# Kernel tuning notes

Hardware: AMD Instinct MI355X
Metric: run time of the kernel (lower is better)

Reference implementation:

```python
import jax, jax.numpy as jnp
import numpy as np

N_NODES = 20000
N_EDGES = 100000
NODE_IN = 16
EDGE_IN = 10
LEAK = 0.1
EPS = 1e-5


def setup_inputs() -> dict:
    key = jax.random.key(0)
    ks = iter(jax.random.split(key, 40))

    def rn(shape, scale):
        return jax.random.normal(next(ks), shape, dtype=jnp.float32) * scale

    inp = {}
    inp["x"] = jax.random.normal(next(ks), (N_NODES, NODE_IN), dtype=jnp.float32)
    inp["e"] = jax.random.normal(next(ks), (N_EDGES, EDGE_IN), dtype=jnp.float32)
    inp["edge_index"] = jax.random.randint(next(ks), (2, N_EDGES), 0, N_NODES, dtype=jnp.int64)
    inp["xbatch"] = jnp.zeros((N_NODES,), dtype=jnp.int64)

    # BatchNorm affine params
    inp["bn_node_g"] = jnp.ones((NODE_IN,), jnp.float32)
    inp["bn_node_b"] = jnp.zeros((NODE_IN,), jnp.float32)
    inp["bn_edge_g"] = jnp.ones((EDGE_IN,), jnp.float32)
    inp["bn_edge_b"] = jnp.zeros((EDGE_IN,), jnp.float32)

    # nn1: Lin(10,16) -> LeakyReLU -> Lin(16, 16*32) -> LeakyReLU
    inp["nn1_w1"] = rn((EDGE_IN, 16), 0.3); inp["nn1_b1"] = jnp.zeros((16,), jnp.float32)
    inp["nn1_w2"] = rn((16, 16 * 32), 0.25); inp["nn1_b2"] = jnp.zeros((16 * 32,), jnp.float32)
    # nn2: Lin(10,32) -> LeakyReLU -> Lin(32, 32*64) -> LeakyReLU
    inp["nn2_w1"] = rn((EDGE_IN, 32), 0.3); inp["nn2_b1"] = jnp.zeros((32,), jnp.float32)
    inp["nn2_w2"] = rn((32, 32 * 64), 0.18); inp["nn2_b2"] = jnp.zeros((32 * 64,), jnp.float32)

    # NNConv root weights + biases
    inp["l1_root"] = rn((16, 32), 0.25); inp["l1_bias"] = jnp.zeros((32,), jnp.float32)
    inp["l2_root"] = rn((32, 64), 0.18); inp["l2_bias"] = jnp.zeros((64,), jnp.float32)

    # edge_pred_mlp: 138 -> 64 -> 32 -> 16 -> 8 -> 2
    dims = [2 * 64 + EDGE_IN, 64, 32, 16, 8, 2]
    for i in range(5):
        inp[f"mlp_w{i+1}"] = rn((dims[i], dims[i + 1]), 1.0 / np.sqrt(dims[i]))
        inp[f"mlp_b{i+1}"] = jnp.zeros((dims[i + 1],), jnp.float32)
    return inp


def _bn(v, g, b):
    # BatchNorm1d, training-mode batch statistics (biased variance), eps=1e-5
    m = v.mean(axis=0)
    var = v.var(axis=0)
    return (v - m) * jax.lax.rsqrt(var + EPS) * g + b


def _lrelu(v):
    return jax.nn.leaky_relu(v, LEAK)


def _nnconv(x, src, dst, e, w1, b1, w2, b2, root, bias, c_in, c_out):
    # edge MLP -> per-edge weight matrix [E, c_in, c_out]
    h = _lrelu(e @ w1 + b1)
    W = _lrelu(h @ w2 + b2).reshape(-1, c_in, c_out)
    # gather source features, per-edge matmul, scatter-add to targets
    msg = jnp.einsum("ei,eio->eo", x[src], W)
    agg = jax.ops.segment_sum(msg, dst, num_segments=x.shape[0])
    return agg + x @ root + bias


def reference(x, e, edge_index, xbatch,
              bn_node_g, bn_node_b, bn_edge_g, bn_edge_b,
              nn1_w1, nn1_b1, nn1_w2, nn1_b2,
              nn2_w1, nn2_b1, nn2_w2, nn2_b2,
              l1_root, l1_bias, l2_root, l2_bias,
              mlp_w1, mlp_b1, mlp_w2, mlp_b2, mlp_w3, mlp_b3,
              mlp_w4, mlp_b4, mlp_w5, mlp_b5):
    src, dst = edge_index[0], edge_index[1]
    e = _bn(e, bn_edge_g, bn_edge_b)
    x = _bn(x, bn_node_g, bn_node_b)
    x = _nnconv(x, src, dst, e, nn1_w1, nn1_b1, nn1_w2, nn1_b2, l1_root, l1_bias, 16, 32)
    x = _nnconv(x, src, dst, e, nn2_w1, nn2_b1, nn2_w2, nn2_b2, l2_root, l2_bias, 32, 64)
    # MetaLayer edge model: cat(source, target, edge_attr) -> MLP -> [E, 2]
    h = jnp.concatenate([x[src], x[dst], e], axis=1)
    h = _lrelu(h @ mlp_w1 + mlp_b1)
    h = _lrelu(h @ mlp_w2 + mlp_b2)
    h = _lrelu(h @ mlp_w3 + mlp_b3)
    h = _lrelu(h @ mlp_w4 + mlp_b4)
    edge_pred = h @ mlp_w5 + mlp_b5
    return edge_pred
```

## Files before the change

kernel.cpp:

```cpp
#include <hip/hip_runtime.h>
#include <cstdint>

#define N_NODES 20000
#define N_EDGES 100000
#define BN_EPS 1e-5f

typedef __attribute__((ext_vector_type(8))) short short8;
typedef __attribute__((ext_vector_type(4))) float floatx4;
typedef __attribute__((ext_vector_type(2))) float float2v;

__device__ __forceinline__ float lrelu(float v) { return fmaxf(v, 0.1f * v); }
__device__ __forceinline__ float4 ld4(const float* p) { return *reinterpret_cast<const float4*>(p); }
__device__ __forceinline__ float2 ld2(const float* p) { return *reinterpret_cast<const float2*>(p); }

__device__ __forceinline__ void atomAddF(float* p, float v) {
#if defined(__HIP_DEVICE_COMPILE__)
    unsafeAtomicAdd(p, v);
#else
    atomicAdd(p, v);
#endif
}

__device__ __forceinline__ unsigned short f2bf(float f) {
    union { float f; uint32_t u; } v; v.f = f;
    uint32_t r = v.u + 0x7fffu + ((v.u >> 16) & 1u);
    return (unsigned short)(r >> 16);
}
__device__ __forceinline__ uint32_t pack2(float a, float b) {
    return (uint32_t)f2bf(a) | ((uint32_t)f2bf(b) << 16);
}
__device__ __forceinline__ short8 pack8(float4 a, float4 b) {
    union { short8 s; uint32_t u[4]; } r;
    r.u[0] = pack2(a.x, a.y); r.u[1] = pack2(a.z, a.w);
    r.u[2] = pack2(b.x, b.y); r.u[3] = pack2(b.z, b.w);
    return r.s;
}

__device__ void stats10_dev(const float* __restrict__ v, int rows, float* __restrict__ out,
                            int blk, int nblk, float* sh) {
    if (threadIdx.x < 20) sh[threadIdx.x] = 0.f;
    __syncthreads();
    int nf2 = rows * 5;
    int stride = nblk * 256;
    int g = blk * 256 + threadIdx.x;
    int c2 = g % 5;
    float s0 = 0.f, s1 = 0.f, q0 = 0.f, q1 = 0.f;
    const float2* p = reinterpret_cast<const float2*>(v);
    for (int i = g; i < nf2; i += stride) {
        float2 t = p[i];
        s0 += t.x; s1 += t.y; q0 += t.x * t.x; q1 += t.y * t.y;
    }
    atomicAdd(&sh[2 * c2], s0);
    atomicAdd(&sh[2 * c2 + 1], s1);
    atomicAdd(&sh[10 + 2 * c2], q0);
    atomicAdd(&sh[10 + 2 * c2 + 1], q1);
    __syncthreads();
    if (threadIdx.x < 20) atomAddF(&out[threadIdx.x], sh[threadIdx.x]);
}

__device__ void stats16_dev(const float* __restrict__ v, int rows, float* __restrict__ out,
                            int blk, int nblk, float* sh) {
    if (threadIdx.x < 32) sh[threadIdx.x] = 0.f;
    __syncthreads();
    int nf4 = rows * 4;
    int stride = nblk * 256;
    int g = blk * 256 + threadIdx.x;
    int cg = (g & 3) * 4;
    float s[4] = {0.f, 0.f, 0.f, 0.f}, q[4] = {0.f, 0.f, 0.f, 0.f};
    const float4* p = reinterpret_cast<const float4*>(v);
    for (int i = g; i < nf4; i += stride) {
        float4 t = p[i];
        s[0] += t.x; s[1] += t.y; s[2] += t.z; s[3] += t.w;
        q[0] += t.x * t.x; q[1] += t.y * t.y; q[2] += t.z * t.z; q[3] += t.w * t.w;
    }
    #pragma unroll
    for (int off = 32; off >= 4; off >>= 1) {
        #pragma unroll
        for (int j = 0; j < 4; ++j) {
            s[j] += __shfl_down(s[j], off, 64);
            q[j] += __shfl_down(q[j], off, 64);
        }
    }
    if ((threadIdx.x & 63) < 4) {
        #pragma unroll
        for (int j = 0; j < 4; ++j) {
            atomicAdd(&sh[cg + j], s[j]);
            atomicAdd(&sh[16 + cg + j], q[j]);
        }
    }
    __syncthreads();
    if (threadIdx.x < 32) atomAddF(&out[threadIdx.x], sh[threadIdx.x]);
}

template<int CIN, int COUT, int H, int OCH>
__device__ void convpack_row(const float* __restrict__ w2, const float* __restrict__ b2,
                             char* __restrict__ pk, int r) {
    constexpr int NROW = CIN * OCH;
    constexpr int WB = NROW * 64;
    constexpr int PACKB = WB + NROW * 4;
    if (r >= CIN * COUT) return;
    int chunk = r / NROW;
    int rem = r % NROW;
    int i = rem / OCH, ol = rem % OCH;
    int n = i * COUT + chunk * OCH + ol;
    char* base = pk + (size_t)chunk * PACKB;
    uint32_t pkv[16];
    #pragma unroll
    for (int t = 0; t < 16; ++t) pkv[t] = 0;
    #pragma unroll
    for (int k = 0; k < H; k += 2)
        pkv[k >> 1] = pack2(w2[(size_t)k * (CIN * COUT) + n],
                            w2[(size_t)(k + 1) * (CIN * COUT) + n]);
    uint4* ob = reinterpret_cast<uint4*>(base);
    #pragma unroll
    for (int q = 0; q < 4; ++q)
        ob[(size_t)q * NROW + rem] = make_uint4(pkv[4 * q], pkv[4 * q + 1],
                                                pkv[4 * q + 2], pkv[4 * q + 3]);
    ((float*)(base + WB))[rem] = b2[n];
}

#define P1_S10 120
#define P1_S16 120
__global__ __launch_bounds__(256)
void prep1_kernel(const float* __restrict__ e, const float* __restrict__ x,
                  float* __restrict__ stats_e, float* __restrict__ stats_x,
                  const int* __restrict__ dst, int* __restrict__ counts,
                  const float* __restrict__ nn1_w2, const float* __restrict__ nn1_b2, char* __restrict__ cpack1,
                  const float* __restrict__ nn2_w2, const float* __restrict__ nn2_b2, char* __restrict__ cpack2,
                  const float* __restrict__ mw1, unsigned short* __restrict__ w1t,
                  const float* __restrict__ mw2, const float* __restrict__ mb2,
                  const float* __restrict__ mw3, const float* __restrict__ mb3,
                  const float* __restrict__ mw4, const float* __restrict__ mb4,
                  const float* __restrict__ mw5, const float* __restrict__ mb5,
                  float* __restrict__ mlpw)
{
    __shared__ float sh[32];
    int b = blockIdx.x;
    if (b < P1_S10) {
        stats10_dev(e, N_EDGES, stats_e, b, P1_S10, sh);
    } else if (b < P1_S10 + P1_S16) {
        stats16_dev(x, N_NODES, stats_x, b - P1_S10, P1_S16, sh);
    } else if (b < 631) {
        int i = (b - 240) * 256 + threadIdx.x;
        if (i < N_EDGES) atomicAdd(&counts[dst[i]], 1);
    } else if (b < 633) {
        convpack_row<16, 32, 16, 32>(nn1_w2, nn1_b2, cpack1, (b - 631) * 256 + threadIdx.x);
    } else if (b < 641) {
        convpack_row<32, 64, 32, 16>(nn2_w2, nn2_b2, cpack2, (b - 633) * 256 + threadIdx.x);
    } else {
        if (threadIdx.x < 64) {
            int o = threadIdx.x;
            for (int k = 0; k < 160; k += 2) {
                float a = (k < 138) ? mw1[(size_t)k * 64 + o] : 0.f;
                float c = (k + 1 < 138) ? mw1[(size_t)(k + 1) * 64 + o] : 0.f;
                *reinterpret_cast<uint32_t*>(w1t + (size_t)o * 160 + k) = pack2(a, c);
            }
        }
        for (int i = threadIdx.x; i < 2764; i += 256) {
            float v = 0.f;
            if (i < 2048) v = mw2[i];
            else if (i < 2560) v = mw3[i - 2048];
            else if (i < 2688) v = mw4[i - 2560];
            else if (i < 2704) v = mw5[i - 2688];
            else if (i < 2736) v = mb2[i - 2704];
            else if (i < 2752) v = mb3[i - 2736];
            else if (i < 2760) v = mb4[i - 2752];
            else if (i < 2762) v = mb5[i - 2760];
            mlpw[i] = v;
        }
    }
}

__global__ void scan_kernel(const int* __restrict__ counts, int* __restrict__ starts,
                            int* __restrict__ cursor, int n) {
    __shared__ int wsum[4];
    const int CH = (n + 255) / 256;
    int t = threadIdx.x;
    int lane = t & 63, wv = t >> 6;
    int lo = t * CH, hi = min(lo + CH, n);
    int s = 0;
    for (int i = lo; i < hi; ++i) s += counts[i];
    int v = s;
    #pragma unroll
    for (int off = 1; off < 64; off <<= 1) {
        int u = __shfl_up(v, off, 64);
        if (lane >= off) v += u;
    }
    if (lane == 63) wsum[wv] = v;
    __syncthreads();
    int woff = 0;
    for (int w = 0; w < wv; ++w) woff += wsum[w];
    int acc = woff + v - s;
    for (int i = lo; i < hi; ++i) {
        starts[i] = acc; cursor[i] = acc; acc += counts[i];
    }
}

#define P2_N16 1250
#define P2_SCAT 391
#define P2_HGEN 391
__global__ __launch_bounds__(256)
void prep2_kernel(const float* __restrict__ x, const float* __restrict__ stats_x,
                  const float* __restrict__ bn_node_g, const float* __restrict__ bn_node_b,
                  float* __restrict__ x_n,
                  const int* __restrict__ dst, int* __restrict__ cursor, int* __restrict__ epos,
                  const float* __restrict__ e, const float* __restrict__ stats_e,
                  const float* __restrict__ bn_edge_g, const float* __restrict__ bn_edge_b,
                  float* __restrict__ e_n,
                  const float* __restrict__ w1a, const float* __restrict__ b1a,
                  const float* __restrict__ w1b, const float* __restrict__ b1b,
                  unsigned short* __restrict__ h1, unsigned short* __restrict__ h2)
{
    int b = blockIdx.x;
    if (b < P2_N16) {
        int idx = b * 256 + threadIdx.x;
        if (idx >= N_NODES * 16) return;
        int c = idx & 15;
        float N = (float)N_NODES;
        float m = stats_x[c] / N;
        float var = stats_x[16 + c] / N - m * m;
        float sc = rsqrtf(var + BN_EPS) * bn_node_g[c];
        x_n[idx] = (x[idx] - m) * sc + bn_node_b[c];
    } else if (b < P2_N16 + P2_SCAT) {
        int i = (b - P2_N16) * 256 + threadIdx.x;
        if (i < N_EDGES) {
            int p = atomicAdd(&cursor[dst[i]], 1);
            epos[i] = p;
        }
    } else {
        int eg = (b - P2_N16 - P2_SCAT) * 256 + threadIdx.x;
        if (eg >= N_EDGES) return;
        float ev[10];
        float Ecnt = (float)N_EDGES;
        #pragma unroll
        for (int j = 0; j < 10; ++j) {
            float m = stats_e[j] / Ecnt;
            float var = stats_e[10 + j] / Ecnt - m * m;
            float sc = rsqrtf(var + BN_EPS) * bn_edge_g[j];
            ev[j] = (e[(size_t)eg * 10 + j] - m) * sc + bn_edge_b[j];
            e_n[(size_t)eg * 10 + j] = ev[j];
        }
        {
            uint32_t pk[16];
            #pragma unroll
            for (int t = 0; t < 16; ++t) pk[t] = 0;
            #pragma unroll
            for (int k = 0; k < 16; k += 2) {
                float a0 = b1a[k], a1 = b1a[k + 1];
                #pragma unroll
                for (int j = 0; j < 10; ++j) {
                    a0 += ev[j] * w1a[j * 16 + k];
                    a1 += ev[j] * w1a[j * 16 + k + 1];
                }
                pk[k >> 1] = pack2(lrelu(a0), lrelu(a1));
            }
            uint4* o = reinterpret_cast<uint4*>(h1 + (size_t)eg * 32);
            o[0] = make_uint4(pk[0], pk[1], pk[2], pk[3]);
            o[1] = make_uint4(pk[4], pk[5], pk[6], pk[7]);
            o[2] = make_uint4(pk[8], pk[9], pk[10], pk[11]);
            o[3] = make_uint4(pk[12], pk[13], pk[14], pk[15]);
        }
        {
            uint32_t pk[16];
            #pragma unroll
            for (int k = 0; k < 32; k += 2) {
                float a0 = b1b[k], a1 = b1b[k + 1];
                #pragma unroll
                for (int j = 0; j < 10; ++j) {
                    a0 += ev[j] * w1b[j * 32 + k];
                    a1 += ev[j] * w1b[j * 32 + k + 1];
                }
                pk[k >> 1] = pack2(lrelu(a0), lrelu(a1));
            }
            uint4* o = reinterpret_cast<uint4*>(h2 + (size_t)eg * 32);
            o[0] = make_uint4(pk[0], pk[1], pk[2], pk[3]);
            o[1] = make_uint4(pk[4], pk[5], pk[6], pk[7]);
            o[2] = make_uint4(pk[8], pk[9], pk[10], pk[11]);
            o[3] = make_uint4(pk[12], pk[13], pk[14], pk[15]);
        }
    }
}

template<int CIN, int COUT, int OCH, int NE>
__global__ __launch_bounds__(256, 4)
void conv_lds_kernel(const unsigned short* __restrict__ hbuf,
                     const char* __restrict__ pack,
                     const int* __restrict__ src,
                     const int* __restrict__ epos,
                     const float* __restrict__ xin,
                     float* __restrict__ msgbuf,
                     int n_edges)
{
    constexpr int NCH = COUT / OCH;
    constexpr int NROW = CIN * OCH;
    constexpr int WB = NROW * 64;
    constexpr int PACKB = WB + NROW * 4;
    __shared__ char smem[PACKB];

    int tid = threadIdx.x;
    int chunk = blockIdx.x % NCH;
    int eblk = blockIdx.x / NCH;

    {
        const uint4* g = reinterpret_cast<const uint4*>(pack + (size_t)chunk * PACKB);
        uint4* s = reinterpret_cast<uint4*>(smem);
        #pragma unroll 1
        for (int o = tid; o < PACKB / 16; o += 256) s[o] = g[o];
    }
    __syncthreads();

    int wv = tid >> 6, lane = tid & 63;
    int el = lane & 15, quad = lane >> 4;
    int g0 = (eblk * 4 + wv) * NE;

    const unsigned short* wlds = reinterpret_cast<const unsigned short*>(smem)
                                 + ((size_t)quad * NROW + el) * 8;
    const float* blds = reinterpret_cast<const float*>(smem + WB) + quad * 4;

    const float2v pt = {0.1f, 0.1f};

    #pragma unroll 1
    for (int gI = 0; gI < NE; ++gI) {
        int e0 = (g0 + gI) * 16;
        if (e0 >= n_edges) return;
        int e = e0 + el;
        int s = src[e];
        int slot = epos[e];

        short8 bfrag = *reinterpret_cast<const short8*>(hbuf + (size_t)e * 32 + quad * 8);

        float xr[CIN];
        #pragma unroll
        for (int i = 0; i < CIN; i += 4) {
            float4 v = ld4(xin + (size_t)s * CIN + i);
            xr[i] = v.x; xr[i + 1] = v.y; xr[i + 2] = v.z; xr[i + 3] = v.w;
        }

        float2v msg0[OCH / 16], msg1[OCH / 16];
        #pragma unroll
        for (int t = 0; t < OCH / 16; ++t) {
            msg0[t] = (float2v){0.f, 0.f};
            msg1[t] = (float2v){0.f, 0.f};
        }

        #pragma unroll 8
        for (int i = 0; i < CIN; ++i) {
            float2v xi2 = {xr[i], xr[i]};
            #pragma unroll
            for (int ot = 0; ot < OCH / 16; ++ot) {
                short8 af = *reinterpret_cast<const short8*>(wlds + (i * OCH + ot * 16) * 8);
                float4 bb = *reinterpret_cast<const float4*>(blds + i * OCH + ot * 16);
                floatx4 c = {bb.x, bb.y, bb.z, bb.w};
                c = __builtin_amdgcn_mfma_f32_16x16x32_bf16(af, bfrag, c, 0, 0, 0);
                float2v c0 = {c[0], c[1]};
                float2v c1 = {c[2], c[3]};
                float2v m0 = __builtin_elementwise_max(c0, c0 * pt);
                float2v m1 = __builtin_elementwise_max(c1, c1 * pt);
                msg0[ot] += xi2 * m0;
                msg1[ot] += xi2 * m1;
            }
        }

        float* orow = msgbuf + (size_t)slot * COUT + chunk * OCH;
        #pragma unroll
        for (int ot = 0; ot < OCH / 16; ++ot)
            *reinterpret_cast<float4*>(orow + ot * 16 + quad * 4) =
                make_float4(msg0[ot][0], msg0[ot][1], msg1[ot][0], msg1[ot][1]);
    }
}

template<int CIN, int C>
__global__ __launch_bounds__(256)
void gather_root_kernel(const float* __restrict__ xin, const float* __restrict__ w,
                        const float* __restrict__ bias,
                        const float* __restrict__ msg,
                        const int* __restrict__ starts, const int* __restrict__ counts,
                        float* __restrict__ xout, int nodes)
{
    constexpr int NPW = 64 / C;
    int wv = blockIdx.x * 4 + (threadIdx.x >> 6);
    int lane = threadIdx.x & 63;
    int node = wv * NPW + lane / C;
    int ch = lane % C;
    if (node >= nodes) return;
    float acc = bias[ch];
    const float* xrow = xin + (size_t)node * CIN;
    #pragma unroll
    for (int i = 0; i < CIN; ++i) acc += xrow[i] * w[i * C + ch];
    int s0 = starts[node], cnt = counts[node];
    const float* mrow = msg + (size_t)s0 * C + ch;
    int i = 0;
    for (; i + 3 < cnt; i += 4) {
        float m0 = mrow[(size_t)(i)     * C];
        float m1 = mrow[(size_t)(i + 1) * C];
        float m2 = mrow[(size_t)(i + 2) * C];
        float m3 = mrow[(size_t)(i + 3) * C];
        acc += (m0 + m1) + (m2 + m3);
    }
    for (; i < cnt; ++i) acc += mrow[(size_t)i * C];
    xout[(size_t)node * C + ch] = acc;
}

__global__ __launch_bounds__(256)
void mlp2_kernel(const float* __restrict__ x2, const float* __restrict__ e_n,
                 const int* __restrict__ src, const int* __restrict__ dst,
                 const unsigned short* __restrict__ w1t, const float* __restrict__ b1,
                 const float* __restrict__ mlpw,
                 float* __restrict__ out, int n_edges)
{
    __shared__ float wl[2764];
    __shared__ float a1t[4 * 1092];
    __shared__ float a2scr[4 * 528];

    int tid = threadIdx.x;
    {
        const uint4* g = reinterpret_cast<const uint4*>(mlpw);
        uint4* s = reinterpret_cast<uint4*>(wl);
        #pragma unroll 1
        for (int i = tid; i < 691; i += 256) s[i] = g[i];
    }

    int wv = tid >> 6, lane = tid & 63;
    int el = lane & 15, quad = lane >> 4;
    int e = blockIdx.x * 64 + wv * 16 + el;
    int eS = (e < n_edges) ? e : (n_edges - 1);
    int sN = src[eS], dN = dst[eS];

    short8 bf[5];
    {
        const float* rs = x2 + (size_t)sN * 64 + quad * 8;
        const float* rd = x2 + (size_t)dN * 64 + quad * 8;
        bf[0] = pack8(ld4(rs), ld4(rs + 4));
        bf[1] = pack8(ld4(rs + 32), ld4(rs + 36));
        bf[2] = pack8(ld4(rd), ld4(rd + 4));
        bf[3] = pack8(ld4(rd + 32), ld4(rd + 36));
        union { short8 s; uint32_t u[4]; } t;
        t.u[0] = t.u[1] = t.u[2] = t.u[3] = 0;
        const float* ep = e_n + (size_t)eS * 10;
        if (quad == 0) {
            float2 p0 = ld2(ep), p1 = ld2(ep + 2), p2 = ld2(ep + 4), p3 = ld2(ep + 6);
            t.u[0] = pack2(p0.x, p0.y); t.u[1] = pack2(p1.x, p1.y);
            t.u[2] = pack2(p2.x, p2.y); t.u[3] = pack2(p3.x, p3.y);
        } else if (quad == 1) {
            float2 p4 = ld2(ep + 8);
            t.u[0] = pack2(p4.x, p4.y);
        }
        bf[4] = t.s;
    }

    float* slab = &a1t[wv * 1092];
    {
        floatx4 acc[4];
        #pragma unroll
        for (int ot = 0; ot < 4; ++ot) {
            float4 bb = ld4(b1 + ot * 16 + quad * 4);
            acc[ot] = (floatx4){bb.x, bb.y, bb.z, bb.w};
        }
        #pragma unroll
        for (int ks = 0; ks < 5; ++ks) {
            #pragma unroll
            for (int ot = 0; ot < 4; ++ot) {
                short8 af = *reinterpret_cast<const short8*>(
                    w1t + (size_t)(ot * 16 + el) * 160 + ks * 32 + quad * 8);
                acc[ot] = __builtin_amdgcn_mfma_f32_16x16x32_bf16(af, bf[ks], acc[ot], 0, 0, 0);
            }
        }
        #pragma unroll
        for (int ot = 0; ot < 4; ++ot) {
            #pragma unroll
            for (int r = 0; r < 4; ++r)
                slab[(ot * 16 + quad * 4 + r) * 17 + el] = lrelu(acc[ot][r]);
        }
    }
    __syncthreads();

    const float* w2l = wl;            const float* w3l = wl + 2048;
    const float* w4l = wl + 2560;     const float* w5l = wl + 2688;
    const float* b2l = wl + 2704;     const float* b3l = wl + 2736;
    const float* b4l = wl + 2752;     const float* b5l = wl + 2760;
    float* a2s = &a2scr[wv * 528];
    float* a3s = slab;
    float* a4s = slab + 512;
    int p = quad;

    {
        float a2[8];
        #pragma unroll
        for (int j = 0; j < 8; ++j) a2[j] = b2l[p * 8 + j];
        #pragma unroll 4
        for (int i = 0; i < 64; ++i) {
            float ai = slab[i * 17 + el];
            #pragma unroll
            for (int j = 0; j < 8; ++j) a2[j] += ai * w2l[i * 32 + p * 8 + j];
        }
        #pragma unroll
        for (int j = 0; j < 8; ++j) a2s[el * 33 + p * 8 + j] = lrelu(a2[j]);
    }
    {
        float a3[4];
        #pragma unroll
        for (int j = 0; j < 4; ++j) a3[j] = b3l[p * 4 + j];
        #pragma unroll 4
        for (int i = 0; i < 32; ++i) {
            float ai = a2s[el * 33 + i];
            #pragma unroll
            for (int j = 0; j < 4; ++j) a3[j] += ai * w3l[i * 16 + p * 4 + j];
        }
        #pragma unroll
        for (int j = 0; j < 4; ++j) a3s[el * 17 + p * 4 + j] = lrelu(a3[j]);
    }
    {
        float a4[2];
        a4[0] = b4l[p * 2]; a4[1] = b4l[p * 2 + 1];
        #pragma unroll
        for (int i = 0; i < 16; ++i) {
            float ai = a3s[el * 17 + i];
            a4[0] += ai * w4l[i * 8 + p * 2];
            a4[1] += ai * w4l[i * 8 + p * 2 + 1];
        }
        a4s[el * 9 + p * 2]     = lrelu(a4[0]);
        a4s[el * 9 + p * 2 + 1] = lrelu(a4[1]);
    }
    if (p < 2) {
        float o = b5l[p];
        #pragma unroll
        for (int i = 0; i < 8; ++i) o += a4s[el * 9 + i] * w5l[i * 2 + p];
        if (e < n_edges) out[(size_t)e * 2 + p] = o;
    }
}

extern "C" void kernel_launch(void* const* d_in, const int* in_sizes, int n_in,
                              void* d_out, int out_size, void* d_ws, size_t ws_size,
                              hipStream_t stream)
{
    const float* x  = (const float*)d_in[0];
    const float* e  = (const float*)d_in[1];
    const int*   ei = (const int*)d_in[2];
    const float* bn_node_g = (const float*)d_in[4];
    const float* bn_node_b = (const float*)d_in[5];
    const float* bn_edge_g = (const float*)d_in[6];
    const float* bn_edge_b = (const float*)d_in[7];
    const float* nn1_w1 = (const float*)d_in[8];
    const float* nn1_b1 = (const float*)d_in[9];
    const float* nn1_w2 = (const float*)d_in[10];
    const float* nn1_b2 = (const float*)d_in[11];
    const float* nn2_w1 = (const float*)d_in[12];
    const float* nn2_b1 = (const float*)d_in[13];
    const float* nn2_w2 = (const float*)d_in[14];
    const float* nn2_b2 = (const float*)d_in[15];
    const float* l1_root = (const float*)d_in[16];
    const float* l1_bias = (const float*)d_in[17];
    const float* l2_root = (const float*)d_in[18];
    const float* l2_bias = (const float*)d_in[19];
    const float* mw1 = (const float*)d_in[20]; const float* mb1 = (const float*)d_in[21];
    const float* mw2 = (const float*)d_in[22]; const float* mb2 = (const float*)d_in[23];
    const float* mw3 = (const float*)d_in[24]; const float* mb3 = (const float*)d_in[25];
    const float* mw4 = (const float*)d_in[26]; const float* mb4 = (const float*)d_in[27];
    const float* mw5 = (const float*)d_in[28]; const float* mb5 = (const float*)d_in[29];

    const int* src = ei;
    const int* dst = ei + N_EDGES;

    float* ws = (float*)d_ws;
    float* stats_e = ws;
    float* stats_x = ws + 32;
    int* counts = (int*)(ws + 64);
    int* starts = counts + 20000;
    int* cursor = starts + 20000;
    int* epos   = cursor + 20000;
    float* e_n = ws + 64 + 160000;
    float* x_n = e_n + 1000000;
    float* x1  = x_n + 320000;
    float* x2  = x1 + 640000;
    float* msg = x2 + 1280000;
    unsigned short* h1   = (unsigned short*)(msg + 6400000);
    unsigned short* h2   = h1 + 3200000;
    unsigned short* w1t  = h2 + 3200000;
    char* cpack1 = (char*)(w1t + 10240);
    char* cpack2 = cpack1 + 34816;
    float* mlpw = (float*)(cpack2 + 4 * 34816);
    float* out = (float*)d_out;

    (void)hipMemsetAsync(d_ws, 0, (64 + 20000) * 4, stream);

    prep1_kernel<<<642, 256, 0, stream>>>(
        e, x, stats_e, stats_x, dst, counts,
        nn1_w2, nn1_b2, cpack1, nn2_w2, nn2_b2, cpack2,
        mw1, w1t, mw2, mb2, mw3, mb3, mw4, mb4, mw5, mb5, mlpw);

    scan_kernel<<<1, 256, 0, stream>>>(counts, starts, cursor, N_NODES);

    prep2_kernel<<<P2_N16 + P2_SCAT + P2_HGEN, 256, 0, stream>>>(
        x, stats_x, bn_node_g, bn_node_b, x_n,
        dst, cursor, epos,
        e, stats_e, bn_edge_g, bn_edge_b, e_n,
        nn1_w1, nn1_b1, nn2_w1, nn2_b1, h1, h2);

    const int NGRP = (N_EDGES + 15) / 16;
    const int CB = (NGRP + 15) / 16;

    conv_lds_kernel<16, 32, 32, 4><<<CB, 256, 0, stream>>>(h1, cpack1, src, epos, x_n, msg, N_EDGES);
    gather_root_kernel<16, 32><<<(N_NODES / 2 + 3) / 4, 256, 0, stream>>>(
        x_n, l1_root, l1_bias, msg, starts, counts, x1, N_NODES);

    conv_lds_kernel<32, 64, 16, 4><<<CB * 4, 256, 0, stream>>>(h2, cpack2, src, epos, x1, msg, N_EDGES);
    gather_root_kernel<32, 64><<<(N_NODES + 3) / 4, 256, 0, stream>>>(
        x1, l2_root, l2_bias, msg, starts, counts, x2, N_NODES);

    mlp2_kernel<<<(N_EDGES + 63) / 64, 256, 0, stream>>>(
        x2, e_n, src, dst, w1t, mb1, mlpw, out, N_EDGES);
}
```

Baseline: 336.1 us.

## Interchange conv loop to reuse LDS weight fragments across edge groups

The per-edge conv kernel now processes all NE edge groups of a wave together. Each LDS weight/bias fragment is loaded once and fed to NE independent MFMAs instead of being reloaded per group. Source indices, slots and h fragments are preloaded up front, and node features are fetched in IB-sized blocks. This cuts LDS traffic and exposes more independent MFMA work, but raises register pressure under the 4-blocks-per-CU launch bound.

```diff
diff --git a/kernel.cpp b/kernel.cpp
--- a/kernel.cpp
+++ b/kernel.cpp
@@ -281,7 +281,7 @@
     }
 }
 
-template<int CIN, int COUT, int OCH, int NE>
+template<int CIN, int COUT, int OCH, int NE, int IB>
 __global__ __launch_bounds__(256, 4)
 void conv_lds_kernel(const unsigned short* __restrict__ hbuf,
                      const char* __restrict__ pack,
@@ -295,6 +295,7 @@
     constexpr int NROW = CIN * OCH;
     constexpr int WB = NROW * 64;
     constexpr int PACKB = WB + NROW * 4;
+    constexpr int NOT = OCH / 16;
     __shared__ char smem[PACKB];
 
     int tid = threadIdx.x;
@@ -312,60 +313,75 @@
     int wv = tid >> 6, lane = tid & 63;
     int el = lane & 15, quad = lane >> 4;
     int g0 = (eblk * 4 + wv) * NE;
+    if (g0 * 16 >= n_edges) return;
 
     const unsigned short* wlds = reinterpret_cast<const unsigned short*>(smem)
                                  + ((size_t)quad * NROW + el) * 8;
     const float* blds = reinterpret_cast<const float*>(smem + WB) + quad * 4;
 
+    int sg[NE], slot[NE];
+    short8 bfrag[NE];
+    #pragma unroll
+    for (int g = 0; g < NE; ++g) {
+        int e0 = (g0 + g) * 16;
+        int e = (e0 < n_edges) ? (e0 + el) : el;
+        sg[g] = src[e];
+        slot[g] = epos[e];
+        bfrag[g] = *reinterpret_cast<const short8*>(hbuf + (size_t)e * 32 + quad * 8);
+    }
+
+    float2v msg0[NE][NOT], msg1[NE][NOT];
+    #pragma unroll
+    for (int g = 0; g < NE; ++g)
+        #pragma unroll
+        for (int t = 0; t < NOT; ++t) {
+            msg0[g][t] = (float2v){0.f, 0.f};
+            msg1[g][t] = (float2v){0.f, 0.f};
+        }
+
     const float2v pt = {0.1f, 0.1f};
 
     #pragma unroll 1
-    for (int gI = 0; gI < NE; ++gI) {
-        int e0 = (g0 + gI) * 16;
-        if (e0 >= n_edges) return;
-        int e = e0 + el;
-        int s = src[e];
-        int slot = epos[e];
-
-        short8 bfrag = *reinterpret_cast<const short8*>(hbuf + (size_t)e * 32 + quad * 8);
-
-        float xr[CIN];
-        #pragma unroll
-        for (int i = 0; i < CIN; i += 4) {
-            float4 v = ld4(xin + (size_t)s * CIN + i);
-            xr[i] = v.x; xr[i + 1] = v.y; xr[i + 2] = v.z; xr[i + 3] = v.w;
-        }
-
-        float2v msg0[OCH / 16], msg1[OCH / 16];
-        #pragma unroll
-        for (int t = 0; t < OCH / 16; ++t) {
-            msg0[t] = (float2v){0.f, 0.f};
-            msg1[t] = (float2v){0.f, 0.f};
-        }
-
-        #pragma unroll 8
-        for (int i = 0; i < CIN; ++i) {
-            float2v xi2 = {xr[i], xr[i]};
-            #pragma unroll
-            for (int ot = 0; ot < OCH / 16; ++ot) {
+    for (int ib = 0; ib < CIN / IB; ++ib) {
+        float xs[NE][IB];
+        #pragma unroll
+        for (int g = 0; g < NE; ++g) {
+            #pragma unroll
+            for (int t = 0; t < IB; t += 4) {
+                float4 v = ld4(xin + (size_t)sg[g] * CIN + ib * IB + t);
+                xs[g][t] = v.x; xs[g][t + 1] = v.y; xs[g][t + 2] = v.z; xs[g][t + 3] = v.w;
+            }
+        }
+        #pragma unroll
+        for (int ii = 0; ii < IB; ++ii) {
+            int i = ib * IB + ii;
+            #pragma unroll
+            for (int ot = 0; ot < NOT; ++ot) {
                 short8 af = *reinterpret_cast<const short8*>(wlds + (i * OCH + ot * 16) * 8);
                 float4 bb = *reinterpret_cast<const float4*>(blds + i * OCH + ot * 16);
-                floatx4 c = {bb.x, bb.y, bb.z, bb.w};
-                c = __builtin_amdgcn_mfma_f32_16x16x32_bf16(af, bfrag, c, 0, 0, 0);
-                float2v c0 = {c[0], c[1]};
-                float2v c1 = {c[2], c[3]};
-                float2v m0 = __builtin_elementwise_max(c0, c0 * pt);
-                float2v m1 = __builtin_elementwise_max(c1, c1 * pt);
-                msg0[ot] += xi2 * m0;
-                msg1[ot] += xi2 * m1;
+                floatx4 cinit = {bb.x, bb.y, bb.z, bb.w};
+                #pragma unroll
+                for (int g = 0; g < NE; ++g) {
+                    floatx4 c = __builtin_amdgcn_mfma_f32_16x16x32_bf16(af, bfrag[g], cinit, 0, 0, 0);
+                    float2v c0 = {c[0], c[1]}, c1 = {c[2], c[3]};
+                    float2v m0 = __builtin_elementwise_max(c0, c0 * pt);
+                    float2v m1 = __builtin_elementwise_max(c1, c1 * pt);
+                    float2v xi2 = {xs[g][ii], xs[g][ii]};
+                    msg0[g][ot] += xi2 * m0;
+                    msg1[g][ot] += xi2 * m1;
+                }
             }
         }
-
-        float* orow = msgbuf + (size_t)slot * COUT + chunk * OCH;
-        #pragma unroll
-        for (int ot = 0; ot < OCH / 16; ++ot)
+    }
+
+    #pragma unroll
+    for (int g = 0; g < NE; ++g) {
+        if ((g0 + g) * 16 >= n_edges) break;
+        float* orow = msgbuf + (size_t)slot[g] * COUT + chunk * OCH;
+        #pragma unroll
+        for (int ot = 0; ot < NOT; ++ot)
             *reinterpret_cast<float4*>(orow + ot * 16 + quad * 4) =
-                make_float4(msg0[ot][0], msg0[ot][1], msg1[ot][0], msg1[ot][1]);
+                make_float4(msg0[g][ot][0], msg0[g][ot][1], msg1[g][ot][0], msg1[g][ot][1]);
     }
 }
 
@@ -599,11 +615,11 @@
     const int NGRP = (N_EDGES + 15) / 16;
     const int CB = (NGRP + 15) / 16;
 
-    conv_lds_kernel<16, 32, 32, 4><<<CB, 256, 0, stream>>>(h1, cpack1, src, epos, x_n, msg, N_EDGES);
+    conv_lds_kernel<16, 32, 32, 4, 4><<<CB, 256, 0, stream>>>(h1, cpack1, src, epos, x_n, msg, N_EDGES);
     gather_root_kernel<16, 32><<<(N_NODES / 2 + 3) / 4, 256, 0, stream>>>(
         x_n, l1_root, l1_bias, msg, starts, counts, x1, N_NODES);
 
-    conv_lds_kernel<32, 64, 16, 4><<<CB * 4, 256, 0, stream>>>(h2, cpack2, src, epos, x1, msg, N_EDGES);
+    conv_lds_kernel<32, 64, 16, 4, 8><<<CB * 4, 256, 0, stream>>>(h2, cpack2, src, epos, x1, msg, N_EDGES);
     gather_root_kernel<32, 64><<<(N_NODES + 3) / 4, 256, 0, stream>>>(
         x1, l2_root, l2_bias, msg, starts, counts, x2, N_NODES);
 
```

Measured after the change: 331.3 us. No clear change (-1.5%).
